# Performance work log

Measured on AMD Instinct MI355X. Metric: run time of the kernel, lower is better.

## Reference

```python
import jax, jax.numpy as jnp
import numpy as np

V, D, H, L, E, DH, K, PMAX = 50257, 128, 4, 4, 8, 512, 2, 256
B, T = 8, 256


def setup_inputs() -> dict:
    key = jax.random.key(0)
    ks = jax.random.split(key, 10)
    s = 0.02
    def n(k, shape):
        return jax.random.normal(k, shape, jnp.float32) * s
    return dict(
        idx=jax.random.randint(ks[0], (B, T), 0, V),
        tok_emb=n(ks[1], (V, D)),
        pos_emb=n(ks[2], (PMAX, D)),
        ln1_g=jnp.ones((L, D), jnp.float32), ln1_b=jnp.zeros((L, D), jnp.float32),
        in_w=n(ks[3], (L, 3 * D, D)), in_b=jnp.zeros((L, 3 * D), jnp.float32),
        out_w=n(ks[4], (L, D, D)), out_b=jnp.zeros((L, D), jnp.float32),
        ln2_g=jnp.ones((L, D), jnp.float32), ln2_b=jnp.zeros((L, D), jnp.float32),
        gate_w=n(ks[5], (L, E, D)),
        w1=n(ks[6], (L, E, DH, D)),
        w2=n(ks[7], (L, E, D, DH)),
        lnf_g=jnp.ones((D,), jnp.float32), lnf_b=jnp.zeros((D,), jnp.float32),
        lm_w=n(ks[8], (V, D)),
    )


def _ln(x, g, b):
    mu = x.mean(-1, keepdims=True)
    var = jnp.var(x, -1, keepdims=True)
    return (x - mu) / jnp.sqrt(var + 1e-5) * g + b


def _moe(x, gw, w1, w2):
    # x: [N, D]; top-2 sparse MoE, computed densely per expert then combined.
    logits = x @ gw.T                              # [N, E]
    probs = jax.nn.softmax(logits, -1)
    topw, topi = jax.lax.top_k(probs, K)           # [N, K]
    topw = topw / topw.sum(-1, keepdims=True)
    we = (topw[..., None] * jax.nn.one_hot(topi, E, dtype=x.dtype)).sum(1)  # [N, E]
    h = jax.nn.silu(jnp.einsum('nd,ehd->neh', x, w1))   # [N, E, DH]
    y = jnp.einsum('neh,edh->ned', h, w2)               # [N, E, D]
    return jnp.einsum('ned,ne->nd', y, we)


def reference(idx, tok_emb, pos_emb, ln1_g, ln1_b, in_w, in_b, out_w, out_b,
              ln2_g, ln2_b, gate_w, w1, w2, lnf_g, lnf_b, lm_w):
    b, t = idx.shape
    x = tok_emb[idx] + pos_emb[:t]                 # [B, T, D]
    dh = D // H
    scale = 1.0 / np.sqrt(dh)
    for l in range(L):
        xl = _ln(x, ln1_g[l], ln1_b[l])
        qkv = xl @ in_w[l].T + in_b[l]
        q, k, v = jnp.split(qkv, 3, -1)
        q = q.reshape(b, t, H, dh)
        k = k.reshape(b, t, H, dh)
        v = v.reshape(b, t, H, dh)
        att = jax.nn.softmax(jnp.einsum('bqhd,bkhd->bhqk', q, k) * scale, -1)
        o = jnp.einsum('bhqk,bkhd->bqhd', att, v).reshape(b, t, D)
        x = x + o @ out_w[l].T + out_b[l]
        x2 = _ln(x, ln2_g[l], ln2_b[l]).reshape(b * t, D)
        x = x + _moe(x2, gate_w[l], w1[l], w2[l]).reshape(b, t, D)
    return _ln(x, lnf_g, lnf_b) @ lm_w.T           # [B, T, V]
```

## Files before the change

### kernel.cpp

```cpp
#include <hip/hip_runtime.h>
#include <math.h>

#define NTOK 2048
#define DD   128
#define NHEAD 4
#define DHEAD 32
#define NLAYER 4
#define NEXP 8
#define DHID 512
#define NVOCAB 50257
#define VPAD  50304
#define SEQ   256
#define NBATCH 8

typedef __attribute__((ext_vector_type(8))) short short8v;
typedef __attribute__((ext_vector_type(4))) float f32x4;

__device__ __forceinline__ unsigned short nm_bf16r(float f) {
  unsigned u = __float_as_uint(f);
  u += 0x7fffu + ((u >> 16) & 1u);
  return (unsigned short)(u >> 16);
}

__device__ __forceinline__ float nm_silu(float a) {
  return a / (1.f + __expf(-a));
}

template<int N4>
__device__ __forceinline__ float nm_dotv(const float* __restrict__ a,
                                         const float* __restrict__ w) {
  const float4* a4 = (const float4*)a;
  const float4* w4 = (const float4*)w;
  float sx = 0.f, sy = 0.f, sz = 0.f, sw = 0.f;
#pragma unroll 16
  for (int k = 0; k < N4; ++k) {
    float4 av = a4[k], wv = w4[k];
    sx = fmaf(av.x, wv.x, sx);
    sy = fmaf(av.y, wv.y, sy);
    sz = fmaf(av.z, wv.z, sz);
    sw = fmaf(av.w, wv.w, sw);
  }
  return (sx + sy) + (sz + sw);
}

__global__ void nm_embed_ln(const int* __restrict__ idx, const float* __restrict__ tok,
                            const float* __restrict__ pos, const float* __restrict__ g,
                            const float* __restrict__ b, float* __restrict__ x,
                            float* __restrict__ xlf, unsigned short* __restrict__ xlb) {
  int n = blockIdx.x, lane = threadIdx.x;
  int t = idx[n];
  float v0 = tok[(size_t)t * DD + lane]      + pos[(n % SEQ) * DD + lane];
  float v1 = tok[(size_t)t * DD + lane + 64] + pos[(n % SEQ) * DD + lane + 64];
  x[n * DD + lane]      = v0;
  x[n * DD + lane + 64] = v1;
  float s = v0 + v1;
#pragma unroll
  for (int o = 32; o > 0; o >>= 1) s += __shfl_xor(s, o, 64);
  float mu = s * (1.f / 128.f);
  float d0 = v0 - mu, d1 = v1 - mu;
  float q = d0 * d0 + d1 * d1;
#pragma unroll
  for (int o = 32; o > 0; o >>= 1) q += __shfl_xor(q, o, 64);
  float rstd = rsqrtf(q * (1.f / 128.f) + 1e-5f);
  float o0 = d0 * rstd * g[lane]      + b[lane];
  float o1 = d1 * rstd * g[lane + 64] + b[lane + 64];
  if (xlf) { xlf[n * DD + lane] = o0; xlf[n * DD + lane + 64] = o1; }
  if (xlb) { xlb[n * DD + lane] = nm_bf16r(o0); xlb[n * DD + lane + 64] = nm_bf16r(o1); }
}

__global__ void nm_ln(const float* __restrict__ in, const float* __restrict__ g,
                      const float* __restrict__ b, float* __restrict__ out) {
  int n = blockIdx.x, lane = threadIdx.x;
  float v0 = in[n * DD + lane], v1 = in[n * DD + lane + 64];
  float s = v0 + v1;
#pragma unroll
  for (int o = 32; o > 0; o >>= 1) s += __shfl_xor(s, o, 64);
  float mu = s * (1.f / 128.f);
  float d0 = v0 - mu, d1 = v1 - mu;
  float q = d0 * d0 + d1 * d1;
#pragma unroll
  for (int o = 32; o > 0; o >>= 1) q += __shfl_xor(q, o, 64);
  float rstd = rsqrtf(q * (1.f / 128.f) + 1e-5f);
  out[n * DD + lane]      = d0 * rstd * g[lane]      + b[lane];
  out[n * DD + lane + 64] = d1 * rstd * g[lane + 64] + b[lane + 64];
}

__global__ void nm_combine_ln(const float* __restrict__ yb, const int* __restrict__ posm,
                              const float* __restrict__ topw, float* __restrict__ x,
                              const float* __restrict__ g, const float* __restrict__ b,
                              float* __restrict__ xl, unsigned short* __restrict__ xb) {
  int n = blockIdx.x, lane = threadIdx.x;
  float w0 = topw[2 * n], w1 = topw[2 * n + 1];
  int p0 = posm[2 * n], p1 = posm[2 * n + 1];
  float v0 = x[n * DD + lane]      + w0 * yb[(size_t)p0 * DD + lane]
                                   + w1 * yb[(size_t)p1 * DD + lane];
  float v1 = x[n * DD + lane + 64] + w0 * yb[(size_t)p0 * DD + lane + 64]
                                   + w1 * yb[(size_t)p1 * DD + lane + 64];
  x[n * DD + lane]      = v0;
  x[n * DD + lane + 64] = v1;
  float s = v0 + v1;
#pragma unroll
  for (int o = 32; o > 0; o >>= 1) s += __shfl_xor(s, o, 64);
  float mu = s * (1.f / 128.f);
  float d0 = v0 - mu, d1 = v1 - mu;
  float q = d0 * d0 + d1 * d1;
#pragma unroll
  for (int o = 32; o > 0; o >>= 1) q += __shfl_xor(q, o, 64);
  float rstd = rsqrtf(q * (1.f / 128.f) + 1e-5f);
  float o0 = d0 * rstd * g[lane]      + b[lane];
  float o1 = d1 * rstd * g[lane + 64] + b[lane + 64];
  xl[n * DD + lane]      = o0;
  xl[n * DD + lane + 64] = o1;
  if (xb) {
    xb[n * DD + lane]      = nm_bf16r(o0);
    xb[n * DD + lane + 64] = nm_bf16r(o1);
  }
}

template<int F>
__global__ __launch_bounds__(256) void nm_gemm2(
    const float* __restrict__ A, const float* __restrict__ B,
    float* __restrict__ C, const float* __restrict__ bias,
    int M, int N, int K,
    const int* __restrict__ list, const int* __restrict__ cnt,
    const int* __restrict__ off) {
  constexpr bool GA = F & 1, SI = F & 2, BI = F & 4, GR = F & 16;
  __shared__ __align__(16) float As[64][132];
  __shared__ __align__(16) float Bs[64][68];
  int tid = threadIdx.x;
  int n0 = blockIdx.x * 64, m0 = blockIdx.y * 128;
  int Mloc = M, o = 0;
  const float* Bb = B;
  if constexpr (GR) {
    int e = blockIdx.z;
    Mloc = cnt[e];
    if (m0 >= Mloc) return;
    o = off[e];
    Bb = B + (size_t)e * (size_t)N * K;
  }
  int tm = tid & 15, tn = tid >> 4;
  float acc[8][4] = {};
  for (int kc = 0; kc < K; kc += 64) {
#pragma unroll
    for (int i = 0; i < 8; ++i) {
      int f = tid + 256 * i;
      int r = f >> 4, c4 = f & 15;
      int mi = m0 + r;
      if (mi >= Mloc) mi = m0;
      const float* ar;
      if constexpr (GA) ar = A + (size_t)(list[o + mi] >> 1) * K;
      else              ar = A + (size_t)(o + mi) * K;
      float4 v = *(const float4*)(ar + kc + c4 * 4);
      int k = c4 * 4;
      As[k][r] = v.x; As[k + 1][r] = v.y; As[k + 2][r] = v.z; As[k + 3][r] = v.w;
    }
#pragma unroll
    for (int i = 0; i < 4; ++i) {
      int f = tid + 256 * i;
      int r = f >> 4, c4 = f & 15;
      const float* br = Bb + (size_t)(n0 + r) * K + kc + c4 * 4;
      float4 v = *(const float4*)br;
      int k = c4 * 4;
      Bs[k][r] = v.x; Bs[k + 1][r] = v.y; Bs[k + 2][r] = v.z; Bs[k + 3][r] = v.w;
    }
    __syncthreads();
#pragma unroll 16
    for (int k = 0; k < 64; ++k) {
      float4 a0 = *(const float4*)&As[k][tm * 4];
      float4 a1 = *(const float4*)&As[k][64 + tm * 4];
      float4 b = *(const float4*)&Bs[k][tn * 4];
      acc[0][0] = fmaf(a0.x, b.x, acc[0][0]); acc[0][1] = fmaf(a0.x, b.y, acc[0][1]);
      acc[0][2] = fmaf(a0.x, b.z, acc[0][2]); acc[0][3] = fmaf(a0.x, b.w, acc[0][3]);
      acc[1][0] = fmaf(a0.y, b.x, acc[1][0]); acc[1][1] = fmaf(a0.y, b.y, acc[1][1]);
      acc[1][2] = fmaf(a0.y, b.z, acc[1][2]); acc[1][3] = fmaf(a0.y, b.w, acc[1][3]);
      acc[2][0] = fmaf(a0.z, b.x, acc[2][0]); acc[2][1] = fmaf(a0.z, b.y, acc[2][1]);
      acc[2][2] = fmaf(a0.z, b.z, acc[2][2]); acc[2][3] = fmaf(a0.z, b.w, acc[2][3]);
      acc[3][0] = fmaf(a0.w, b.x, acc[3][0]); acc[3][1] = fmaf(a0.w, b.y, acc[3][1]);
      acc[3][2] = fmaf(a0.w, b.z, acc[3][2]); acc[3][3] = fmaf(a0.w, b.w, acc[3][3]);
      acc[4][0] = fmaf(a1.x, b.x, acc[4][0]); acc[4][1] = fmaf(a1.x, b.y, acc[4][1]);
      acc[4][2] = fmaf(a1.x, b.z, acc[4][2]); acc[4][3] = fmaf(a1.x, b.w, acc[4][3]);
      acc[5][0] = fmaf(a1.y, b.x, acc[5][0]); acc[5][1] = fmaf(a1.y, b.y, acc[5][1]);
      acc[5][2] = fmaf(a1.y, b.z, acc[5][2]); acc[5][3] = fmaf(a1.y, b.w, acc[5][3]);
      acc[6][0] = fmaf(a1.z, b.x, acc[6][0]); acc[6][1] = fmaf(a1.z, b.y, acc[6][1]);
      acc[6][2] = fmaf(a1.z, b.z, acc[6][2]); acc[6][3] = fmaf(a1.z, b.w, acc[6][3]);
      acc[7][0] = fmaf(a1.w, b.x, acc[7][0]); acc[7][1] = fmaf(a1.w, b.y, acc[7][1]);
      acc[7][2] = fmaf(a1.w, b.z, acc[7][2]); acc[7][3] = fmaf(a1.w, b.w, acc[7][3]);
    }
    __syncthreads();
  }
  float4 bv = {0.f, 0.f, 0.f, 0.f};
  if constexpr (BI) bv = *(const float4*)(bias + n0 + tn * 4);
#pragma unroll
  for (int g = 0; g < 2; ++g) {
#pragma unroll
    for (int i = 0; i < 4; ++i) {
      int row = m0 + g * 64 + tm * 4 + i;
      if (GR && row >= Mloc) continue;
      float* cr = C + (size_t)(o + row) * N + n0 + tn * 4;
      float r0 = acc[g * 4 + i][0], r1 = acc[g * 4 + i][1];
      float r2 = acc[g * 4 + i][2], r3 = acc[g * 4 + i][3];
      if constexpr (BI) { r0 += bv.x; r1 += bv.y; r2 += bv.z; r3 += bv.w; }
      if constexpr (SI) { r0 = nm_silu(r0); r1 = nm_silu(r1); r2 = nm_silu(r2); r3 = nm_silu(r3); }
      float4 st = {r0, r1, r2, r3};
      *(float4*)cr = st;
    }
  }
}

template<int F, int KK>
__global__ __launch_bounds__(256) void nm_bgemm(
    const unsigned short* __restrict__ A, const unsigned short* __restrict__ B,
    float* __restrict__ Cf, unsigned short* __restrict__ Cb,
    const float* __restrict__ bias, int M, int N,
    const int* __restrict__ list, const int* __restrict__ cnt,
    const int* __restrict__ off) {
  constexpr bool GA = F & 1, SI = F & 2, BI = F & 4, SB = F & 8, GR = F & 16;
  int wave = threadIdx.x >> 6, lane = threadIdx.x & 63;
  int n0 = blockIdx.x * 32;
  int m0 = blockIdx.y * 128 + wave * 32;
  int Mloc = M, o = 0;
  const unsigned short* Bb = B;
  if constexpr (GR) {
    int e = blockIdx.z;
    Mloc = cnt[e];
    o = off[e];
    Bb = B + (size_t)e * (size_t)N * KK;
  }
  if (m0 >= Mloc) return;
  int lr = lane & 15, lk = (lane >> 4) * 8;
  const unsigned short* arow[2];
#pragma unroll
  for (int i = 0; i < 2; ++i) {
    int mi = m0 + i * 16 + lr;
    if (mi >= Mloc) mi = Mloc - 1;
    int r = GA ? (list[o + mi] >> 1) : (o + mi);
    arow[i] = A + (size_t)r * KK;
  }
  const unsigned short* brow[2] = { Bb + (size_t)(n0 + lr) * KK,
                                    Bb + (size_t)(n0 + 16 + lr) * KK };
  f32x4 acc[2][2] = {};
#pragma unroll
  for (int ks = 0; ks < KK / 32; ++ks) {
    int kb = ks * 32 + lk;
    short8v a0 = *(const short8v*)(arow[0] + kb);
    short8v a1 = *(const short8v*)(arow[1] + kb);
    short8v b0 = *(const short8v*)(brow[0] + kb);
    short8v b1 = *(const short8v*)(brow[1] + kb);
    acc[0][0] = __builtin_amdgcn_mfma_f32_16x16x32_bf16(a0, b0, acc[0][0], 0, 0, 0);
    acc[0][1] = __builtin_amdgcn_mfma_f32_16x16x32_bf16(a0, b1, acc[0][1], 0, 0, 0);
    acc[1][0] = __builtin_amdgcn_mfma_f32_16x16x32_bf16(a1, b0, acc[1][0], 0, 0, 0);
    acc[1][1] = __builtin_amdgcn_mfma_f32_16x16x32_bf16(a1, b1, acc[1][1], 0, 0, 0);
  }
  float bc[2] = {0.f, 0.f};
  if constexpr (BI) {
    bc[0] = bias[n0 + (lane & 15)];
    bc[1] = bias[n0 + 16 + (lane & 15)];
  }
#pragma unroll
  for (int i = 0; i < 2; ++i) {
    int rbase = m0 + i * 16 + (lane >> 4) * 4;
#pragma unroll
    for (int r = 0; r < 4; ++r) {
      int row = rbase + r;
      if (GR && row >= Mloc) continue;
#pragma unroll
      for (int j = 0; j < 2; ++j) {
        float v = acc[i][j][r];
        if constexpr (BI) v += bc[j];
        if constexpr (SI) v = nm_silu(v);
        int col = n0 + j * 16 + (lane & 15);
        if constexpr (SB) Cb[(size_t)(o + row) * N + col] = nm_bf16r(v);
        else              Cf[(size_t)(o + row) * N + col] = v;
      }
    }
  }
}

__global__ __launch_bounds__(256) void nm_oplng(
    const float* __restrict__ ao, const float* __restrict__ w,
    const float* __restrict__ bias, float* __restrict__ x,
    const float* __restrict__ g, const float* __restrict__ b,
    float* __restrict__ xlf, unsigned short* __restrict__ xlb,
    const float* __restrict__ gw,
    int* __restrict__ topi, float* __restrict__ topw, int* __restrict__ cnt) {
  __shared__ __align__(16) float As[64][36];
  __shared__ __align__(16) float Bs[64][132];
  __shared__ float Ls[32][9];
  int tid = threadIdx.x;
  int m0 = blockIdx.x * 32;
  int tm = tid >> 5, tn = tid & 31;
  float acc[4][4] = {};
  for (int kc = 0; kc < DD; kc += 64) {
#pragma unroll
    for (int i = 0; i < 2; ++i) {
      int ch = tid + 256 * i, r = ch >> 4, c4 = ch & 15;
      float4 v = *(const float4*)(ao + (size_t)(m0 + r) * DD + kc + c4 * 4);
      int k = c4 * 4;
      As[k][r] = v.x; As[k + 1][r] = v.y; As[k + 2][r] = v.z; As[k + 3][r] = v.w;
    }
#pragma unroll
    for (int i = 0; i < 8; ++i) {
      int ch = tid + 256 * i, r = ch >> 4, c4 = ch & 15;
      float4 v = *(const float4*)(w + (size_t)r * DD + kc + c4 * 4);
      int k = c4 * 4;
      Bs[k][r] = v.x; Bs[k + 1][r] = v.y; Bs[k + 2][r] = v.z; Bs[k + 3][r] = v.w;
    }
    __syncthreads();
#pragma unroll 8
    for (int k = 0; k < 64; ++k) {
      float4 a = *(const float4*)&As[k][tm * 4];
      float4 bb = *(const float4*)&Bs[k][tn * 4];
      acc[0][0] = fmaf(a.x, bb.x, acc[0][0]); acc[0][1] = fmaf(a.x, bb.y, acc[0][1]);
      acc[0][2] = fmaf(a.x, bb.z, acc[0][2]); acc[0][3] = fmaf(a.x, bb.w, acc[0][3]);
      acc[1][0] = fmaf(a.y, bb.x, acc[1][0]); acc[1][1] = fmaf(a.y, bb.y, acc[1][1]);
      acc[1][2] = fmaf(a.y, bb.z, acc[1][2]); acc[1][3] = fmaf(a.y, bb.w, acc[1][3]);
      acc[2][0] = fmaf(a.z, bb.x, acc[2][0]); acc[2][1] = fmaf(a.z, bb.y, acc[2][1]);
      acc[2][2] = fmaf(a.z, bb.z, acc[2][2]); acc[2][3] = fmaf(a.z, bb.w, acc[2][3]);
      acc[3][0] = fmaf(a.w, bb.x, acc[3][0]); acc[3][1] = fmaf(a.w, bb.y, acc[3][1]);
      acc[3][2] = fmaf(a.w, bb.z, acc[3][2]); acc[3][3] = fmaf(a.w, bb.w, acc[3][3]);
    }
    __syncthreads();
  }
  float4 bv = *(const float4*)(bias + tn * 4);
  float rr[4][4], s1[4], s2[4];
#pragma unroll
  for (int i = 0; i < 4; ++i) {
    int rw = m0 + tm * 4 + i;
    float4 xv = *(const float4*)(x + (size_t)rw * DD + tn * 4);
    float r0 = acc[i][0] + bv.x + xv.x;
    float r1 = acc[i][1] + bv.y + xv.y;
    float r2 = acc[i][2] + bv.z + xv.z;
    float r3 = acc[i][3] + bv.w + xv.w;
    rr[i][0] = r0; rr[i][1] = r1; rr[i][2] = r2; rr[i][3] = r3;
    float4 st = {r0, r1, r2, r3};
    *(float4*)(x + (size_t)rw * DD + tn * 4) = st;
    s1[i] = r0 + r1 + r2 + r3;
    s2[i] = r0 * r0 + r1 * r1 + r2 * r2 + r3 * r3;
  }
#pragma unroll
  for (int o = 16; o >= 1; o >>= 1) {
#pragma unroll
    for (int i = 0; i < 4; ++i) {
      s1[i] += __shfl_xor(s1[i], o, 64);
      s2[i] += __shfl_xor(s2[i], o, 64);
    }
  }
  float4 gv  = *(const float4*)(g + tn * 4);
  float4 bbv = *(const float4*)(b + tn * 4);
#pragma unroll
  for (int i = 0; i < 4; ++i) {
    int rw = m0 + tm * 4 + i;
    float mu = s1[i] * (1.f / 128.f);
    float var = s2[i] * (1.f / 128.f) - mu * mu;
    float rstd = rsqrtf(var + 1e-5f);
    float y0 = (rr[i][0] - mu) * rstd * gv.x + bbv.x;
    float y1 = (rr[i][1] - mu) * rstd * gv.y + bbv.y;
    float y2 = (rr[i][2] - mu) * rstd * gv.z + bbv.z;
    float y3 = (rr[i][3] - mu) * rstd * gv.w + bbv.w;
    float4 yv = {y0, y1, y2, y3};
    if (xlf) *(float4*)(xlf + (size_t)rw * DD + tn * 4) = yv;
    if (xlb) {
      ushort4 us = {nm_bf16r(y0), nm_bf16r(y1), nm_bf16r(y2), nm_bf16r(y3)};
      *(ushort4*)(xlb + (size_t)rw * DD + tn * 4) = us;
    }
    *(float4*)&Bs[tm * 4 + i][tn * 4] = yv;
  }
  __syncthreads();
  int grow = tid >> 3, ge = tid & 7;
  const float4* xr = (const float4*)&Bs[grow][0];
  const float4* wr = (const float4*)(gw + (size_t)ge * DD);
  float sx = 0.f, sy = 0.f, sz = 0.f, sw = 0.f;
#pragma unroll
  for (int k2 = 0; k2 < 32; ++k2) {
    float4 a = xr[k2], w4 = wr[k2];
    sx = fmaf(a.x, w4.x, sx); sy = fmaf(a.y, w4.y, sy);
    sz = fmaf(a.z, w4.z, sz); sw = fmaf(a.w, w4.w, sw);
  }
  Ls[grow][ge] = (sx + sy) + (sz + sw);
  __syncthreads();
  if (ge == 0) {
    float gl[NEXP];
#pragma unroll
    for (int e = 0; e < NEXP; ++e) gl[e] = Ls[grow][e];
    int i0 = 0;
#pragma unroll
    for (int e = 1; e < NEXP; ++e) if (gl[e] > gl[i0]) i0 = e;
    int i1 = (i0 == 0) ? 1 : 0;
#pragma unroll
    for (int e = 0; e < NEXP; ++e) { if (e != i0 && gl[e] > gl[i1]) i1 = e; }
    float p1 = __expf(gl[i1] - gl[i0]);
    float inv = 1.f / (1.f + p1);
    int n = m0 + grow;
    topi[2 * n] = i0; topi[2 * n + 1] = i1;
    topw[2 * n] = inv; topw[2 * n + 1] = p1 * inv;
    atomicAdd(cnt + i0, 1);
    atomicAdd(cnt + i1, 1);
  }
}

__global__ __launch_bounds__(256) void nm_attn2(const float* __restrict__ qkv,
                                                float* __restrict__ o) {
  __shared__ __align__(16) float Ks[SEQ][DHEAD];
  __shared__ __align__(16) float Vs[SEQ][DHEAD];
  __shared__ float mbuf[32][9], sbuf[32][9];
  __shared__ __align__(16) float accbuf[32][36];
  int bh = blockIdx.x;
  int b = bh >> 2, h = bh & 3;
  int qt = blockIdx.y;
  int tid = threadIdx.x;
  const float* base = qkv + (size_t)b * SEQ * 384;
  for (int f = tid; f < SEQ * 8; f += 256) {
    int t = f >> 3, c4 = f & 7;
    float4 kv = *(const float4*)(base + (size_t)t * 384 + 128 + h * DHEAD + c4 * 4);
    float4 vv = *(const float4*)(base + (size_t)t * 384 + 256 + h * DHEAD + c4 * 4);
    *(float4*)&Ks[t][c4 * 4] = kv;
    *(float4*)&Vs[t][c4 * 4] = vv;
  }
  __syncthreads();
  int q = tid & 31, slot = tid >> 5;
  int tq = qt * 32 + q;
  float qv[DHEAD];
  const float4* q4 = (const float4*)(base + (size_t)tq * 384 + h * DHEAD);
#pragma unroll
  for (int k = 0; k < 8; ++k) {
    float4 v = q4[k];
    qv[4*k] = v.x; qv[4*k+1] = v.y; qv[4*k+2] = v.z; qv[4*k+3] = v.w;
  }
  float m = -1e30f, s = 0.f, acc[DHEAD];
#pragma unroll
  for (int d = 0; d < DHEAD; ++d) acc[d] = 0.f;
  const float scale = 0.17677669529663687f;
  int j0 = slot * 32;
  for (int jj = 0; jj < 32; ++jj) {
    int j = j0 + jj;
    const float4* kr = (const float4*)Ks[j];
    float sc = 0.f;
#pragma unroll
    for (int k = 0; k < 8; ++k) {
      float4 v = kr[k];
      sc += qv[4*k]*v.x + qv[4*k+1]*v.y + qv[4*k+2]*v.z + qv[4*k+3]*v.w;
    }
    sc *= scale;
    float mn = fmaxf(m, sc);
    float f = __expf(m - mn), p = __expf(sc - mn);
    s = s * f + p;
    const float4* vr = (const float4*)Vs[j];
#pragma unroll
    for (int k = 0; k < 8; ++k) {
      float4 v = vr[k];
      acc[4*k]   = acc[4*k]  * f + p * v.x;
      acc[4*k+1] = acc[4*k+1]* f + p * v.y;
      acc[4*k+2] = acc[4*k+2]* f + p * v.z;
      acc[4*k+3] = acc[4*k+3]* f + p * v.w;
    }
    m = mn;
  }
  mbuf[q][slot] = m;
  sbuf[q][slot] = s;
  __syncthreads();
  float M = mbuf[q][0];
#pragma unroll
  for (int t = 1; t < 8; ++t) M = fmaxf(M, mbuf[q][t]);
  float S = 0.f;
#pragma unroll
  for (int t = 0; t < 8; ++t) S += sbuf[q][t] * __expf(mbuf[q][t] - M);
  float w = __expf(m - M);
#pragma unroll
  for (int d = 0; d < DHEAD; ++d) acc[d] *= w;
#pragma unroll
  for (int p = 0; p < 8; ++p) {
    if (slot == p) {
      if (p == 0) {
#pragma unroll
        for (int d = 0; d < DHEAD; ++d) accbuf[q][d] = acc[d];
      } else {
#pragma unroll
        for (int d = 0; d < DHEAD; ++d) accbuf[q][d] += acc[d];
      }
    }
    __syncthreads();
  }
  if (slot == 0) sbuf[q][8] = 1.f / S;
  __syncthreads();
  int q2 = tid >> 3, c4 = tid & 7;
  float inv = sbuf[q2][8];
  float4 v = *(const float4*)&accbuf[q2][c4 * 4];
  v.x *= inv; v.y *= inv; v.z *= inv; v.w *= inv;
  *(float4*)(o + (size_t)(b * SEQ + qt * 32 + q2) * DD + h * DHEAD + c4 * 4) = v;
}

__global__ void nm_route(const int* __restrict__ topi, const int* __restrict__ cnt,
                         int* __restrict__ off, int* __restrict__ list,
                         int* __restrict__ posm) {
  __shared__ int lcur[NEXP];
  int tid = threadIdx.x;
  if (tid < NEXP) {
    int o = 0;
    for (int e = 0; e < tid; ++e) o += cnt[e];
    lcur[tid] = o;
    off[tid] = o;
  }
  __syncthreads();
  for (int t = tid; t < 2 * NTOK; t += 1024) {
    int e = topi[t];
    int p = atomicAdd(&lcur[e], 1);
    list[p] = t;
    posm[t] = p;
  }
}

__global__ void nm_zero(int* __restrict__ p, int n) {
  int i = blockIdx.x * 64 + threadIdx.x;
  if (i < n) p[i] = 0;
}

#define C3_LMW 6438912ull
#define C3_W1  6963200ull
#define C3_ALL 7487488ull
__global__ void nm_cvt3(const float* __restrict__ lmw, const float* __restrict__ w1l3,
                        const float* __restrict__ w2l3,
                        unsigned short* __restrict__ lmwb,
                        unsigned short* __restrict__ w1b3,
                        unsigned short* __restrict__ w2b3) {
  size_t i = (size_t)blockIdx.x * 256 + threadIdx.x;
  if (i < C3_LMW) {
    lmwb[i] = (i < (size_t)NVOCAB * DD) ? nm_bf16r(lmw[i]) : (unsigned short)0;
  } else if (i < C3_W1) {
    size_t j = i - C3_LMW; w1b3[j] = nm_bf16r(w1l3[j]);
  } else if (i < C3_ALL) {
    size_t j = i - C3_W1; w2b3[j] = nm_bf16r(w2l3[j]);
  }
}

__global__ void nm_qkv(const float* __restrict__ xl, const float* __restrict__ w,
                       const float* __restrict__ bias, float* __restrict__ qkv) {
  __shared__ __align__(16) float xs[DD];
  int n = blockIdx.x, tid = threadIdx.x;
  xs[tid] = xl[n * DD + tid];
  __syncthreads();
#pragma unroll
  for (int jj = 0; jj < 3; ++jj) {
    int j = tid + jj * 128;
    qkv[(size_t)n * 384 + j] = nm_dotv<32>(xs, w + (size_t)j * DD) + bias[j];
  }
}

__global__ void nm_outproj(const float* __restrict__ ao, const float* __restrict__ w,
                           const float* __restrict__ bias, float* __restrict__ x) {
  __shared__ __align__(16) float os[DD];
  int n = blockIdx.x, tid = threadIdx.x;
  os[tid] = ao[n * DD + tid];
  __syncthreads();
  x[n * DD + tid] += nm_dotv<32>(os, w + (size_t)tid * DD) + bias[tid];
}

__global__ void nm_moe(const float* __restrict__ x2, const float* __restrict__ gw,
                       const float* __restrict__ w1, const float* __restrict__ w2,
                       float* __restrict__ x) {
  __shared__ __align__(16) float xs[DD];
  __shared__ __align__(16) float hs[DHID];
  __shared__ float gl[NEXP];
  __shared__ int   ei[2];
  __shared__ float ew[2];
  int n = blockIdx.x, tid = threadIdx.x;
  if (tid < DD) xs[tid] = x2[n * DD + tid];
  __syncthreads();
  if (tid < NEXP) gl[tid] = nm_dotv<32>(xs, gw + (size_t)tid * DD);
  __syncthreads();
  if (tid == 0) {
    int i0 = 0;
#pragma unroll
    for (int e = 1; e < NEXP; ++e) if (gl[e] > gl[i0]) i0 = e;
    int i1 = (i0 == 0) ? 1 : 0;
    for (int e = 0; e < NEXP; ++e) { if (e == i0) continue; if (gl[e] > gl[i1]) i1 = e; }
    float p1 = __expf(gl[i1] - gl[i0]);
    float inv = 1.f / (1.f + p1);
    ei[0] = i0; ei[1] = i1; ew[0] = inv; ew[1] = p1 * inv;
  }
  __syncthreads();
  float yacc = 0.f;
  for (int t2 = 0; t2 < 2; ++t2) {
    int e = ei[t2];
    float wt = ew[t2];
    const float* w1e = w1 + (size_t)e * DHID * DD;
#pragma unroll
    for (int jj = 0; jj < 2; ++jj) {
      int j = tid + jj * 256;
      float a = nm_dotv<32>(xs, w1e + (size_t)j * DD);
      hs[j] = nm_silu(a);
    }
    __syncthreads();
    if (tid < DD) yacc += wt * nm_dotv<128>(hs, w2 + ((size_t)e * DD + tid) * DHID);
    __syncthreads();
  }
  if (tid < DD) x[n * DD + tid] += yacc;
}

__device__ __forceinline__ short8v nm_cvt8(const float* p) {
  const float4* p4 = (const float4*)p;
  float4 a = p4[0], b = p4[1];
  short8v r;
  r[0] = (short)nm_bf16r(a.x); r[1] = (short)nm_bf16r(a.y);
  r[2] = (short)nm_bf16r(a.z); r[3] = (short)nm_bf16r(a.w);
  r[4] = (short)nm_bf16r(b.x); r[5] = (short)nm_bf16r(b.y);
  r[6] = (short)nm_bf16r(b.z); r[7] = (short)nm_bf16r(b.w);
  return r;
}

__global__ __launch_bounds__(256) void nm_lmhead_f32(
    const float* __restrict__ xf, const float* __restrict__ lmw,
    float* __restrict__ out) {
  int wave = threadIdx.x >> 6, lane = threadIdx.x & 63;
  int wr = wave >> 1, wc = wave & 1;
  int row0 = blockIdx.y * 128 + wr * 64;
  int col0 = blockIdx.x * 128 + wc * 64;
  int lr = lane & 15, lk = (lane >> 4) * 8;
  f32x4 acc[4][4] = {};
#pragma unroll
  for (int ks = 0; ks < 4; ++ks) {
    int kb = ks * 32 + lk;
    short8v a[4], b[4];
#pragma unroll
    for (int i = 0; i < 4; ++i)
      a[i] = nm_cvt8(xf + (size_t)(row0 + i * 16 + lr) * DD + kb);
#pragma unroll
    for (int j = 0; j < 4; ++j) {
      int c = col0 + j * 16 + lr;
      if (c < NVOCAB) b[j] = nm_cvt8(lmw + (size_t)c * DD + kb);
      else {
        short8v z;
#pragma unroll
        for (int e = 0; e < 8; ++e) z[e] = 0;
        b[j] = z;
      }
    }
#pragma unroll
    for (int i = 0; i < 4; ++i)
#pragma unroll
      for (int j = 0; j < 4; ++j)
        acc[i][j] = __builtin_amdgcn_mfma_f32_16x16x32_bf16(a[i], b[j], acc[i][j], 0, 0, 0);
  }
  int cr = (lane >> 4) * 4;
#pragma unroll
  for (int j = 0; j < 4; ++j) {
    int c = col0 + j * 16 + (lane & 15);
    if (c < NVOCAB) {
#pragma unroll
      for (int i = 0; i < 4; ++i)
#pragma unroll
        for (int r = 0; r < 4; ++r)
          out[(size_t)(row0 + i * 16 + cr + r) * NVOCAB + c] = acc[i][j][r];
    }
  }
}

__global__ __launch_bounds__(256) void nm_lmhead2(
    const unsigned short* __restrict__ xfb, const unsigned short* __restrict__ lmwb,
    float* __restrict__ out) {
  __shared__ unsigned short Ab[128 * 128];
  __shared__ unsigned short Bb[128 * 128];
  int tid = threadIdx.x;
  int row0 = blockIdx.y * 128, col0 = blockIdx.x * 128;
#pragma unroll
  for (int i = 0; i < 8; ++i) {
    int ch = tid + i * 256;
    int r = ch >> 4, s = ch & 15;
    int sg = s ^ (r & 7);
    *(short8v*)&Ab[r * 128 + s * 8] =
        *(const short8v*)(xfb + (size_t)(row0 + r) * DD + sg * 8);
    *(short8v*)&Bb[r * 128 + s * 8] =
        *(const short8v*)(lmwb + (size_t)(col0 + r) * DD + sg * 8);
  }
  __syncthreads();
  int wave = tid >> 6, lane = tid & 63;
  int wr = wave >> 1, wc = wave & 1;
  int lr = lane & 15, hk = lane >> 4;
  f32x4 acc[4][4] = {};
#pragma unroll
  for (int ks = 0; ks < 4; ++ks) {
    int sg = ks * 4 + hk;
    int sx = (sg ^ (lr & 7)) * 8;
    short8v a[4], b[4];
#pragma unroll
    for (int i = 0; i < 4; ++i)
      a[i] = *(const short8v*)&Ab[(wr * 64 + i * 16 + lr) * 128 + sx];
#pragma unroll
    for (int j = 0; j < 4; ++j)
      b[j] = *(const short8v*)&Bb[(wc * 64 + j * 16 + lr) * 128 + sx];
#pragma unroll
    for (int i = 0; i < 4; ++i)
#pragma unroll
      for (int j = 0; j < 4; ++j)
        acc[i][j] = __builtin_amdgcn_mfma_f32_16x16x32_bf16(a[i], b[j], acc[i][j], 0, 0, 0);
  }
  int cr = (lane >> 4) * 4;
#pragma unroll
  for (int j = 0; j < 4; ++j) {
    int c = col0 + wc * 64 + j * 16 + (lane & 15);
    if (c < NVOCAB) {
#pragma unroll
      for (int i = 0; i < 4; ++i)
#pragma unroll
        for (int r = 0; r < 4; ++r)
          out[(size_t)(row0 + wr * 64 + i * 16 + cr + r) * NVOCAB + c] = acc[i][j][r];
    }
  }
}

extern "C" void kernel_launch(void* const* d_in, const int* in_sizes, int n_in,
                              void* d_out, int out_size, void* d_ws, size_t ws_size,
                              hipStream_t stream) {
  const int*   idx   = (const int*)  d_in[0];
  const float* tok   = (const float*)d_in[1];
  const float* pos   = (const float*)d_in[2];
  const float* ln1g  = (const float*)d_in[3];
  const float* ln1b  = (const float*)d_in[4];
  const float* inw   = (const float*)d_in[5];
  const float* inb   = (const float*)d_in[6];
  const float* outw  = (const float*)d_in[7];
  const float* outb  = (const float*)d_in[8];
  const float* ln2g  = (const float*)d_in[9];
  const float* ln2b  = (const float*)d_in[10];
  const float* gatew = (const float*)d_in[11];
  const float* w1    = (const float*)d_in[12];
  const float* w2    = (const float*)d_in[13];
  const float* lnfg  = (const float*)d_in[14];
  const float* lnfb  = (const float*)d_in[15];
  const float* lmw   = (const float*)d_in[16];
  float* out = (float*)d_out;

  float* ws   = (float*)d_ws;
  float* x    = ws;
  float* xl   = x    + NTOK * DD;
  float* qkv  = xl   + NTOK * DD;
  float* ao   = qkv  + NTOK * 384;
  float* topw = ao   + NTOK * DD;
  float* H    = topw + 2 * NTOK;
  float* yb   = H    + 2 * NTOK * DHID;
  int*   topi = (int*)(yb + 2 * NTOK * DD);
  int*   list = topi + 2 * NTOK;
  int*   posm = list + 2 * NTOK;
  int*   cnt  = posm + 2 * NTOK;
  int*   offs = cnt  + NLAYER * NEXP;
  unsigned short* xlb  = (unsigned short*)(offs + NLAYER * NEXP);
  unsigned short* Hb   = xlb + NTOK * DD;
  unsigned short* xfb  = Hb  + 2 * NTOK * DHID;
  unsigned short* w1b3 = xfb + NTOK * DD;
  unsigned short* w2b3 = w1b3 + NEXP * DHID * DD;
  unsigned short* lmwb = w2b3 + NEXP * DD * DHID;
  const size_t need = (size_t)((char*)(lmwb + (size_t)VPAD * DD) - (char*)d_ws);
  const bool pre = (ws_size >= need);

  const float* w1l3 = w1 + (size_t)3 * NEXP * DHID * DD;
  const float* w2l3 = w2 + (size_t)3 * NEXP * DD * DHID;

  if (pre) {
    nm_cvt3<<<(unsigned)(C3_ALL / 256), 256, 0, stream>>>(
        lmw, w1l3, w2l3, lmwb, w1b3, w2b3);
    nm_zero<<<1, 64, 0, stream>>>(cnt, NLAYER * NEXP);
    nm_embed_ln<<<NTOK, 64, 0, stream>>>(idx, tok, pos, ln1g, ln1b, x, xl, nullptr);
    for (int l = 0; l < NLAYER; ++l) {
      nm_gemm2<4><<<dim3(384 / 64, NTOK / 128), 256, 0, stream>>>(
          xl, inw + (size_t)l * 384 * DD, qkv, inb + (size_t)l * 384,
          NTOK, 384, DD, nullptr, nullptr, nullptr);
      nm_attn2<<<dim3(NBATCH * NHEAD, SEQ / 32), 256, 0, stream>>>(qkv, ao);
      nm_oplng<<<NTOK / 32, 256, 0, stream>>>(
          ao, outw + (size_t)l * DD * DD, outb + (size_t)l * DD, x,
          ln2g + l * DD, ln2b + l * DD, xl, (l == 3) ? xlb : (unsigned short*)nullptr,
          gatew + (size_t)l * NEXP * DD, topi, topw, cnt + l * NEXP);
      int* cnt_l = cnt + l * NEXP;
      int* off_l = offs + l * NEXP;
      nm_route<<<1, 1024, 0, stream>>>(topi, cnt_l, off_l, list, posm);
      if (l < 3) {
        const float* w1l = w1 + (size_t)l * NEXP * DHID * DD;
        const float* w2l = w2 + (size_t)l * NEXP * DD * DHID;
        nm_gemm2<19><<<dim3(DHID / 64, 2 * NTOK / 128, NEXP), 256, 0, stream>>>(
            xl, w1l, H, nullptr, 0, DHID, DD, list, cnt_l, off_l);
        nm_gemm2<16><<<dim3(DD / 64, 2 * NTOK / 128, NEXP), 256, 0, stream>>>(
            H, w2l, yb, nullptr, 0, DD, DHID, nullptr, cnt_l, off_l);
      } else {
        nm_bgemm<27, 128><<<dim3(DHID / 32, 32, NEXP), 256, 0, stream>>>(
            xlb, w1b3, nullptr, Hb, nullptr, 0, DHID, list, cnt_l, off_l);
        nm_bgemm<16, 512><<<dim3(DD / 32, 32, NEXP), 256, 0, stream>>>(
            Hb, w2b3, yb, nullptr, nullptr, 0, DD, nullptr, cnt_l, off_l);
      }
      const float* gN = (l < NLAYER - 1) ? ln1g + (l + 1) * DD : lnfg;
      const float* bN = (l < NLAYER - 1) ? ln1b + (l + 1) * DD : lnfb;
      nm_combine_ln<<<NTOK, 64, 0, stream>>>(
          yb, posm, topw, x, gN, bN, xl,
          (l == NLAYER - 1) ? xfb : (unsigned short*)nullptr);
    }
    nm_lmhead2<<<dim3(VPAD / 128, NTOK / 128), 256, 0, stream>>>(xfb, lmwb, out);
  } else {
    nm_embed_ln<<<NTOK, 64, 0, stream>>>(idx, tok, pos, ln1g, ln1b, x, xl, nullptr);
    for (int l = 0; l < NLAYER; ++l) {
      nm_qkv<<<NTOK, 128, 0, stream>>>(xl, inw + (size_t)l * 384 * DD,
                                       inb + (size_t)l * 384, qkv);
      nm_attn2<<<dim3(NBATCH * NHEAD, SEQ / 32), 256, 0, stream>>>(qkv, ao);
      nm_outproj<<<NTOK, 128, 0, stream>>>(ao, outw + (size_t)l * DD * DD,
                                           outb + (size_t)l * DD, x);
      nm_ln<<<NTOK, 64, 0, stream>>>(x, ln2g + l * DD, ln2b + l * DD, xl);
      nm_moe<<<NTOK, 256, 0, stream>>>(xl, gatew + (size_t)l * NEXP * DD,
                                       w1 + (size_t)l * NEXP * DHID * DD,
                                       w2 + (size_t)l * NEXP * DD * DHID, x);
      const float* gN = (l < NLAYER - 1) ? ln1g + (l + 1) * DD : lnfg;
      const float* bN = (l < NLAYER - 1) ? ln1b + (l + 1) * DD : lnfb;
      nm_ln<<<NTOK, 64, 0, stream>>>(x, gN, bN, xl);
    }
    nm_lmhead_f32<<<dim3(VPAD / 128, NTOK / 128), 256, 0, stream>>>(xl, lmw, out);
  }
}
```

Baseline: 825.5 us.

## Fuse init kernels, merge routing into oplng, coalesce lm-head stores

```diff
diff --git a/kernel.cpp b/kernel.cpp
--- a/kernel.cpp
+++ b/kernel.cpp
@@ -43,10 +43,67 @@
   return (sx + sy) + (sz + sw);
 }
 
+#define C3_LMW 6438912ull
+#define C3_W1  6963200ull
+#define C3_ALL 7487488ull
+#define CVTB   7312
+__global__ __launch_bounds__(256) void nm_init(
+    const int* __restrict__ idx, const float* __restrict__ tok,
+    const float* __restrict__ pos, const float* __restrict__ g,
+    const float* __restrict__ b, const float* __restrict__ lmw,
+    const float* __restrict__ w1l3, const float* __restrict__ w2l3,
+    float* __restrict__ x, float* __restrict__ xl,
+    unsigned short* __restrict__ lmwb, unsigned short* __restrict__ w1b3,
+    unsigned short* __restrict__ w2b3, int* __restrict__ zp) {
+  int bid = blockIdx.x, tid = threadIdx.x;
+  if (bid < CVTB) {
+    size_t base = ((size_t)bid * 256 + tid) * 4;
+    if (base < (size_t)NVOCAB * DD) {
+      float4 v = *(const float4*)(lmw + base);
+      ushort4 us = {nm_bf16r(v.x), nm_bf16r(v.y), nm_bf16r(v.z), nm_bf16r(v.w)};
+      *(ushort4*)(lmwb + base) = us;
+    } else if (base < C3_LMW) {
+      ushort4 us = {0, 0, 0, 0};
+      *(ushort4*)(lmwb + base) = us;
+    } else if (base < C3_W1) {
+      size_t j = base - C3_LMW;
+      float4 v = *(const float4*)(w1l3 + j);
+      ushort4 us = {nm_bf16r(v.x), nm_bf16r(v.y), nm_bf16r(v.z), nm_bf16r(v.w)};
+      *(ushort4*)(w1b3 + j) = us;
+    } else {
+      size_t j = base - C3_W1;
+      float4 v = *(const float4*)(w2l3 + j);
+      ushort4 us = {nm_bf16r(v.x), nm_bf16r(v.y), nm_bf16r(v.z), nm_bf16r(v.w)};
+      *(ushort4*)(w2b3 + j) = us;
+    }
+  } else if (bid < CVTB + NTOK / 4) {
+    int n = (bid - CVTB) * 4 + (tid >> 6);
+    int lane = tid & 63;
+    int t = idx[n];
+    float v0 = tok[(size_t)t * DD + lane]      + pos[(n % SEQ) * DD + lane];
+    float v1 = tok[(size_t)t * DD + lane + 64] + pos[(n % SEQ) * DD + lane + 64];
+    x[n * DD + lane]      = v0;
+    x[n * DD + lane + 64] = v1;
+    float s = v0 + v1;
+#pragma unroll
+    for (int o = 32; o > 0; o >>= 1) s += __shfl_xor(s, o, 64);
+    float mu = s * (1.f / 128.f);
+    float d0 = v0 - mu, d1 = v1 - mu;
+    float q = d0 * d0 + d1 * d1;
+#pragma unroll
+    for (int o = 32; o > 0; o >>= 1) q += __shfl_xor(q, o, 64);
+    float rstd = rsqrtf(q * (1.f / 128.f) + 1e-5f);
+    xl[n * DD + lane]      = d0 * rstd * g[lane]      + b[lane];
+    xl[n * DD + lane + 64] = d1 * rstd * g[lane + 64] + b[lane + 64];
+  } else {
+    if (tid < 68) zp[tid] = 0;
+  }
+}
+
 __global__ void nm_embed_ln(const int* __restrict__ idx, const float* __restrict__ tok,
                             const float* __restrict__ pos, const float* __restrict__ g,
                             const float* __restrict__ b, float* __restrict__ x,
-                            float* __restrict__ xlf, unsigned short* __restrict__ xlb) {
+                            float* __restrict__ xlf) {
   int n = blockIdx.x, lane = threadIdx.x;
   int t = idx[n];
   float v0 = tok[(size_t)t * DD + lane]      + pos[(n % SEQ) * DD + lane];
@@ -62,10 +119,8 @@
 #pragma unroll
   for (int o = 32; o > 0; o >>= 1) q += __shfl_xor(q, o, 64);
   float rstd = rsqrtf(q * (1.f / 128.f) + 1e-5f);
-  float o0 = d0 * rstd * g[lane]      + b[lane];
-  float o1 = d1 * rstd * g[lane + 64] + b[lane + 64];
-  if (xlf) { xlf[n * DD + lane] = o0; xlf[n * DD + lane + 64] = o1; }
-  if (xlb) { xlb[n * DD + lane] = nm_bf16r(o0); xlb[n * DD + lane + 64] = nm_bf16r(o1); }
+  xlf[n * DD + lane]      = d0 * rstd * g[lane]      + b[lane];
+  xlf[n * DD + lane + 64] = d1 * rstd * g[lane + 64] + b[lane + 64];
 }
 
 __global__ void nm_ln(const float* __restrict__ in, const float* __restrict__ g,
@@ -117,7 +172,7 @@
   }
 }
 
-template<int F>
+template<int F, int MT>
 __global__ __launch_bounds__(256) void nm_gemm2(
     const float* __restrict__ A, const float* __restrict__ B,
     float* __restrict__ C, const float* __restrict__ bias,
@@ -125,10 +180,11 @@
     const int* __restrict__ list, const int* __restrict__ cnt,
     const int* __restrict__ off) {
   constexpr bool GA = F & 1, SI = F & 2, BI = F & 4, GR = F & 16;
-  __shared__ __align__(16) float As[64][132];
+  constexpr int RG = MT / 64;
+  __shared__ __align__(16) float As[64][MT + 4];
   __shared__ __align__(16) float Bs[64][68];
   int tid = threadIdx.x;
-  int n0 = blockIdx.x * 64, m0 = blockIdx.y * 128;
+  int n0 = blockIdx.x * 64, m0 = blockIdx.y * MT;
   int Mloc = M, o = 0;
   const float* Bb = B;
   if constexpr (GR) {
@@ -139,10 +195,10 @@
     Bb = B + (size_t)e * (size_t)N * K;
   }
   int tm = tid & 15, tn = tid >> 4;
-  float acc[8][4] = {};
+  float acc[RG * 4][4] = {};
   for (int kc = 0; kc < K; kc += 64) {
 #pragma unroll
-    for (int i = 0; i < 8; ++i) {
+    for (int i = 0; i < RG * 4; ++i) {
       int f = tid + 256 * i;
       int r = f >> 4, c4 = f & 15;
       int mi = m0 + r;
@@ -166,39 +222,41 @@
     __syncthreads();
 #pragma unroll 16
     for (int k = 0; k < 64; ++k) {
-      float4 a0 = *(const float4*)&As[k][tm * 4];
-      float4 a1 = *(const float4*)&As[k][64 + tm * 4];
       float4 b = *(const float4*)&Bs[k][tn * 4];
-      acc[0][0] = fmaf(a0.x, b.x, acc[0][0]); acc[0][1] = fmaf(a0.x, b.y, acc[0][1]);
-      acc[0][2] = fmaf(a0.x, b.z, acc[0][2]); acc[0][3] = fmaf(a0.x, b.w, acc[0][3]);
-      acc[1][0] = fmaf(a0.y, b.x, acc[1][0]); acc[1][1] = fmaf(a0.y, b.y, acc[1][1]);
-      acc[1][2] = fmaf(a0.y, b.z, acc[1][2]); acc[1][3] = fmaf(a0.y, b.w, acc[1][3]);
-      acc[2][0] = fmaf(a0.z, b.x, acc[2][0]); acc[2][1] = fmaf(a0.z, b.y, acc[2][1]);
-      acc[2][2] = fmaf(a0.z, b.z, acc[2][2]); acc[2][3] = fmaf(a0.z, b.w, acc[2][3]);
-      acc[3][0] = fmaf(a0.w, b.x, acc[3][0]); acc[3][1] = fmaf(a0.w, b.y, acc[3][1]);
-      acc[3][2] = fmaf(a0.w, b.z, acc[3][2]); acc[3][3] = fmaf(a0.w, b.w, acc[3][3]);
-      acc[4][0] = fmaf(a1.x, b.x, acc[4][0]); acc[4][1] = fmaf(a1.x, b.y, acc[4][1]);
-      acc[4][2] = fmaf(a1.x, b.z, acc[4][2]); acc[4][3] = fmaf(a1.x, b.w, acc[4][3]);
-      acc[5][0] = fmaf(a1.y, b.x, acc[5][0]); acc[5][1] = fmaf(a1.y, b.y, acc[5][1]);
-      acc[5][2] = fmaf(a1.y, b.z, acc[5][2]); acc[5][3] = fmaf(a1.y, b.w, acc[5][3]);
-      acc[6][0] = fmaf(a1.z, b.x, acc[6][0]); acc[6][1] = fmaf(a1.z, b.y, acc[6][1]);
-      acc[6][2] = fmaf(a1.z, b.z, acc[6][2]); acc[6][3] = fmaf(a1.z, b.w, acc[6][3]);
-      acc[7][0] = fmaf(a1.w, b.x, acc[7][0]); acc[7][1] = fmaf(a1.w, b.y, acc[7][1]);
-      acc[7][2] = fmaf(a1.w, b.z, acc[7][2]); acc[7][3] = fmaf(a1.w, b.w, acc[7][3]);
+#pragma unroll
+      for (int g2 = 0; g2 < RG; ++g2) {
+        float4 a = *(const float4*)&As[k][g2 * 64 + tm * 4];
+        acc[g2*4+0][0] = fmaf(a.x, b.x, acc[g2*4+0][0]);
+        acc[g2*4+0][1] = fmaf(a.x, b.y, acc[g2*4+0][1]);
+        acc[g2*4+0][2] = fmaf(a.x, b.z, acc[g2*4+0][2]);
+        acc[g2*4+0][3] = fmaf(a.x, b.w, acc[g2*4+0][3]);
+        acc[g2*4+1][0] = fmaf(a.y, b.x, acc[g2*4+1][0]);
+        acc[g2*4+1][1] = fmaf(a.y, b.y, acc[g2*4+1][1]);
+        acc[g2*4+1][2] = fmaf(a.y, b.z, acc[g2*4+1][2]);
+        acc[g2*4+1][3] = fmaf(a.y, b.w, acc[g2*4+1][3]);
+        acc[g2*4+2][0] = fmaf(a.z, b.x, acc[g2*4+2][0]);
+        acc[g2*4+2][1] = fmaf(a.z, b.y, acc[g2*4+2][1]);
+        acc[g2*4+2][2] = fmaf(a.z, b.z, acc[g2*4+2][2]);
+        acc[g2*4+2][3] = fmaf(a.z, b.w, acc[g2*4+2][3]);
+        acc[g2*4+3][0] = fmaf(a.w, b.x, acc[g2*4+3][0]);
+        acc[g2*4+3][1] = fmaf(a.w, b.y, acc[g2*4+3][1]);
+        acc[g2*4+3][2] = fmaf(a.w, b.z, acc[g2*4+3][2]);
+        acc[g2*4+3][3] = fmaf(a.w, b.w, acc[g2*4+3][3]);
+      }
     }
     __syncthreads();
   }
   float4 bv = {0.f, 0.f, 0.f, 0.f};
   if constexpr (BI) bv = *(const float4*)(bias + n0 + tn * 4);
 #pragma unroll
-  for (int g = 0; g < 2; ++g) {
+  for (int g2 = 0; g2 < RG; ++g2) {
 #pragma unroll
     for (int i = 0; i < 4; ++i) {
-      int row = m0 + g * 64 + tm * 4 + i;
+      int row = m0 + g2 * 64 + tm * 4 + i;
       if (GR && row >= Mloc) continue;
       float* cr = C + (size_t)(o + row) * N + n0 + tn * 4;
-      float r0 = acc[g * 4 + i][0], r1 = acc[g * 4 + i][1];
-      float r2 = acc[g * 4 + i][2], r3 = acc[g * 4 + i][3];
+      float r0 = acc[g2 * 4 + i][0], r1 = acc[g2 * 4 + i][1];
+      float r2 = acc[g2 * 4 + i][2], r3 = acc[g2 * 4 + i][3];
       if constexpr (BI) { r0 += bv.x; r1 += bv.y; r2 += bv.z; r3 += bv.w; }
       if constexpr (SI) { r0 = nm_silu(r0); r1 = nm_silu(r1); r2 = nm_silu(r2); r3 = nm_silu(r3); }
       float4 st = {r0, r1, r2, r3};
@@ -282,10 +340,14 @@
     const float* __restrict__ g, const float* __restrict__ b,
     float* __restrict__ xlf, unsigned short* __restrict__ xlb,
     const float* __restrict__ gw,
-    int* __restrict__ topi, float* __restrict__ topw, int* __restrict__ cnt) {
+    int* __restrict__ topi, float* __restrict__ topw, int* __restrict__ cnt,
+    int* __restrict__ ticket, int* __restrict__ off, int* __restrict__ list,
+    int* __restrict__ posm) {
   __shared__ __align__(16) float As[64][36];
   __shared__ __align__(16) float Bs[64][132];
   __shared__ float Ls[32][9];
+  __shared__ int doR;
+  __shared__ int cv[NEXP], lcur[NEXP];
   int tid = threadIdx.x;
   int m0 = blockIdx.x * 32;
   int tm = tid >> 5, tn = tid & 31;
@@ -395,6 +457,30 @@
     topw[2 * n] = inv; topw[2 * n + 1] = p1 * inv;
     atomicAdd(cnt + i0, 1);
     atomicAdd(cnt + i1, 1);
+  }
+  __syncthreads();
+  if (tid == 0) {
+    __threadfence();
+    doR = (atomicAdd(ticket, 1) == 63);
+    if (doR) __threadfence();
+  }
+  __syncthreads();
+  if (doR) {
+    if (tid < NEXP) cv[tid] = atomicAdd(cnt + tid, 0);
+    __syncthreads();
+    if (tid < NEXP) {
+      int o2 = 0;
+      for (int e = 0; e < tid; ++e) o2 += cv[e];
+      lcur[tid] = o2;
+      off[tid] = o2;
+    }
+    __syncthreads();
+    for (int t = tid; t < 2 * NTOK; t += 256) {
+      int e = topi[t];
+      int p = atomicAdd(&lcur[e], 1);
+      list[p] = t;
+      posm[t] = p;
+    }
   }
 }
 
@@ -489,49 +575,6 @@
   *(float4*)(o + (size_t)(b * SEQ + qt * 32 + q2) * DD + h * DHEAD + c4 * 4) = v;
 }
 
-__global__ void nm_route(const int* __restrict__ topi, const int* __restrict__ cnt,
-                         int* __restrict__ off, int* __restrict__ list,
-                         int* __restrict__ posm) {
-  __shared__ int lcur[NEXP];
-  int tid = threadIdx.x;
-  if (tid < NEXP) {
-    int o = 0;
-    for (int e = 0; e < tid; ++e) o += cnt[e];
-    lcur[tid] = o;
-    off[tid] = o;
-  }
-  __syncthreads();
-  for (int t = tid; t < 2 * NTOK; t += 1024) {
-    int e = topi[t];
-    int p = atomicAdd(&lcur[e], 1);
-    list[p] = t;
-    posm[t] = p;
-  }
-}
-
-__global__ void nm_zero(int* __restrict__ p, int n) {
-  int i = blockIdx.x * 64 + threadIdx.x;
-  if (i < n) p[i] = 0;
-}
-
-#define C3_LMW 6438912ull
-#define C3_W1  6963200ull
-#define C3_ALL 7487488ull
-__global__ void nm_cvt3(const float* __restrict__ lmw, const float* __restrict__ w1l3,
-                        const float* __restrict__ w2l3,
-                        unsigned short* __restrict__ lmwb,
-                        unsigned short* __restrict__ w1b3,
-                        unsigned short* __restrict__ w2b3) {
-  size_t i = (size_t)blockIdx.x * 256 + threadIdx.x;
-  if (i < C3_LMW) {
-    lmwb[i] = (i < (size_t)NVOCAB * DD) ? nm_bf16r(lmw[i]) : (unsigned short)0;
-  } else if (i < C3_W1) {
-    size_t j = i - C3_LMW; w1b3[j] = nm_bf16r(w1l3[j]);
-  } else if (i < C3_ALL) {
-    size_t j = i - C3_W1; w2b3[j] = nm_bf16r(w2l3[j]);
-  }
-}
-
 __global__ void nm_qkv(const float* __restrict__ xl, const float* __restrict__ w,
                        const float* __restrict__ bias, float* __restrict__ qkv) {
   __shared__ __align__(16) float xs[DD];
@@ -657,8 +700,9 @@
 __global__ __launch_bounds__(256) void nm_lmhead2(
     const unsigned short* __restrict__ xfb, const unsigned short* __restrict__ lmwb,
     float* __restrict__ out) {
-  __shared__ unsigned short Ab[128 * 128];
-  __shared__ unsigned short Bb[128 * 128];
+  __shared__ __align__(16) unsigned char smem[132 * 128 * 4];
+  unsigned short* Ab = (unsigned short*)smem;
+  unsigned short* Bb = Ab + 128 * 128;
   int tid = threadIdx.x;
   int row0 = blockIdx.y * 128, col0 = blockIdx.x * 128;
 #pragma unroll
@@ -693,16 +737,30 @@
       for (int j = 0; j < 4; ++j)
         acc[i][j] = __builtin_amdgcn_mfma_f32_16x16x32_bf16(a[i], b[j], acc[i][j], 0, 0, 0);
   }
-  int cr = (lane >> 4) * 4;
-#pragma unroll
-  for (int j = 0; j < 4; ++j) {
-    int c = col0 + wc * 64 + j * 16 + (lane & 15);
-    if (c < NVOCAB) {
-#pragma unroll
-      for (int i = 0; i < 4; ++i)
-#pragma unroll
-        for (int r = 0; r < 4; ++r)
-          out[(size_t)(row0 + wr * 64 + i * 16 + cr + r) * NVOCAB + c] = acc[i][j][r];
+  __syncthreads();
+  float* Cs = (float*)smem;
+  int hi4 = hk * 4;
+#pragma unroll
+  for (int j = 0; j < 4; ++j)
+#pragma unroll
+    for (int i = 0; i < 4; ++i)
+#pragma unroll
+      for (int r = 0; r < 4; ++r)
+        Cs[(wr * 64 + i * 16 + hi4 + r) * 132 + wc * 64 + j * 16 + lr] = acc[i][j][r];
+  __syncthreads();
+  bool full = (col0 + 128 <= NVOCAB);
+#pragma unroll 4
+  for (int rr = 0; rr < 32; ++rr) {
+    int row = wave * 32 + rr;
+    float v0 = Cs[row * 132 + lane];
+    float v1 = Cs[row * 132 + 64 + lane];
+    size_t base = (size_t)(row0 + row) * NVOCAB + col0;
+    if (full) {
+      out[base + lane] = v0;
+      out[base + 64 + lane] = v1;
+    } else {
+      if (col0 + lane < NVOCAB)      out[base + lane] = v0;
+      if (col0 + 64 + lane < NVOCAB) out[base + 64 + lane] = v1;
     }
   }
 }
@@ -742,7 +800,8 @@
   int*   posm = list + 2 * NTOK;
   int*   cnt  = posm + 2 * NTOK;
   int*   offs = cnt  + NLAYER * NEXP;
-  unsigned short* xlb  = (unsigned short*)(offs + NLAYER * NEXP);
+  int*   tick = offs + NLAYER * NEXP;
+  unsigned short* xlb  = (unsigned short*)(tick + 8);
   unsigned short* Hb   = xlb + NTOK * DD;
   unsigned short* xfb  = Hb  + 2 * NTOK * DHID;
   unsigned short* w1b3 = xfb + NTOK * DD;
@@ -755,28 +814,26 @@
   const float* w2l3 = w2 + (size_t)3 * NEXP * DD * DHID;
 
   if (pre) {
-    nm_cvt3<<<(unsigned)(C3_ALL / 256), 256, 0, stream>>>(
-        lmw, w1l3, w2l3, lmwb, w1b3, w2b3);
-    nm_zero<<<1, 64, 0, stream>>>(cnt, NLAYER * NEXP);
-    nm_embed_ln<<<NTOK, 64, 0, stream>>>(idx, tok, pos, ln1g, ln1b, x, xl, nullptr);
+    nm_init<<<CVTB + NTOK / 4 + 1, 256, 0, stream>>>(
+        idx, tok, pos, ln1g, ln1b, lmw, w1l3, w2l3, x, xl, lmwb, w1b3, w2b3, cnt);
     for (int l = 0; l < NLAYER; ++l) {
-      nm_gemm2<4><<<dim3(384 / 64, NTOK / 128), 256, 0, stream>>>(
+      nm_gemm2<4, 128><<<dim3(384 / 64, NTOK / 128), 256, 0, stream>>>(
           xl, inw + (size_t)l * 384 * DD, qkv, inb + (size_t)l * 384,
           NTOK, 384, DD, nullptr, nullptr, nullptr);
       nm_attn2<<<dim3(NBATCH * NHEAD, SEQ / 32), 256, 0, stream>>>(qkv, ao);
       nm_oplng<<<NTOK / 32, 256, 0, stream>>>(
           ao, outw + (size_t)l * DD * DD, outb + (size_t)l * DD, x,
           ln2g + l * DD, ln2b + l * DD, xl, (l == 3) ? xlb : (unsigned short*)nullptr,
-          gatew + (size_t)l * NEXP * DD, topi, topw, cnt + l * NEXP);
+          gatew + (size_t)l * NEXP * DD, topi, topw, cnt + l * NEXP,
+          tick + l, offs + l * NEXP, list, posm);
       int* cnt_l = cnt + l * NEXP;
       int* off_l = offs + l * NEXP;
-      nm_route<<<1, 1024, 0, stream>>>(topi, cnt_l, off_l, list, posm);
       if (l < 3) {
         const float* w1l = w1 + (size_t)l * NEXP * DHID * DD;
         const float* w2l = w2 + (size_t)l * NEXP * DD * DHID;
-        nm_gemm2<19><<<dim3(DHID / 64, 2 * NTOK / 128, NEXP), 256, 0, stream>>>(
+        nm_gemm2<19, 128><<<dim3(DHID / 64, 2 * NTOK / 128, NEXP), 256, 0, stream>>>(
             xl, w1l, H, nullptr, 0, DHID, DD, list, cnt_l, off_l);
-        nm_gemm2<16><<<dim3(DD / 64, 2 * NTOK / 128, NEXP), 256, 0, stream>>>(
+        nm_gemm2<16, 64><<<dim3(DD / 64, 2 * NTOK / 64, NEXP), 256, 0, stream>>>(
             H, w2l, yb, nullptr, 0, DD, DHID, nullptr, cnt_l, off_l);
       } else {
         nm_bgemm<27, 128><<<dim3(DHID / 32, 32, NEXP), 256, 0, stream>>>(
@@ -792,7 +849,7 @@
     }
     nm_lmhead2<<<dim3(VPAD / 128, NTOK / 128), 256, 0, stream>>>(xfb, lmwb, out);
   } else {
-    nm_embed_ln<<<NTOK, 64, 0, stream>>>(idx, tok, pos, ln1g, ln1b, x, xl, nullptr);
+    nm_embed_ln<<<NTOK, 64, 0, stream>>>(idx, tok, pos, ln1g, ln1b, x, xl);
     for (int l = 0; l < NLAYER; ++l) {
       nm_qkv<<<NTOK, 128, 0, stream>>>(xl, inw + (size_t)l * 384 * DD,
                                        inb + (size_t)l * 384, qkv);
```

Result: no change. 828.4 us (+0.4%).
